# Optimization experiments

Measured on AMD Instinct MI355X. Metric: run time of the kernel, lower is better.

## Reference

```python
import math
import jax, jax.numpy as jnp
import numpy as np

B, T, IN, D, H, L = 128, 1024, 32, 128, 8, 2
U = max(1, min(int(5 * math.log(T + 1)), T))  # ProbSparse sampled queries = 34


def setup_inputs() -> dict:
    key = jax.random.key(0)
    ks = jax.random.split(key, 12)
    def w(k, shape):
        fan_in = shape[-2]
        return jax.random.normal(k, shape, jnp.float32) / jnp.sqrt(jnp.float32(fan_in))
    idx = jnp.stack([jax.random.permutation(jax.random.fold_in(ks[1], l), T)[:U]
                     for l in range(L)]).astype(jnp.int64 if jax.config.jax_enable_x64 else jnp.int32)
    return {
        "x": jax.random.normal(ks[0], (B, T, IN), jnp.float32),
        "idx": idx,
        "proj_w": w(ks[2], (IN, D)), "proj_b": jnp.zeros((D,), jnp.float32),
        "wq": w(ks[3], (L, D, D)), "wk": w(ks[4], (L, D, D)), "wv": w(ks[5], (L, D, D)),
        "wo": w(ks[6], (L, D, D)), "wo_b": jnp.zeros((L, D), jnp.float32),
        "ln1_g": jnp.ones((L, D), jnp.float32), "ln1_b": jnp.zeros((L, D), jnp.float32),
        "ff1_w": w(ks[7], (L, D, 4 * D)), "ff1_b": jnp.zeros((L, 4 * D), jnp.float32),
        "ff2_w": w(ks[8], (L, 4 * D, D)), "ff2_b": jnp.zeros((L, D), jnp.float32),
        "ln2_g": jnp.ones((L, D), jnp.float32), "ln2_b": jnp.zeros((L, D), jnp.float32),
        "head_g": jnp.ones((D,), jnp.float32), "head_bb": jnp.zeros((D,), jnp.float32),
        "head_w": w(ks[9], (D, 1)), "head_wb": jnp.zeros((1,), jnp.float32),
    }


def _ln(x, g, b, eps=1e-5):
    m = x.mean(-1, keepdims=True)
    v = ((x - m) ** 2).mean(-1, keepdims=True)
    return (x - m) / jnp.sqrt(v + eps) * g + b


def _pos_encoding():
    pos = jnp.arange(T, dtype=jnp.float32)[:, None]
    div = jnp.exp(jnp.arange(0, D, 2, dtype=jnp.float32) * (-math.log(10000.0) / D))
    # interleave sin/cos -> [T, D]
    return jnp.stack([jnp.sin(pos * div), jnp.cos(pos * div)], axis=-1).reshape(T, D)


def reference(x, idx, proj_w, proj_b, wq, wk, wv, wo, wo_b, ln1_g, ln1_b,
              ff1_w, ff1_b, ff2_w, ff2_b, ln2_g, ln2_b,
              head_g, head_bb, head_w, head_wb):
    Dh = D // H
    h = x @ proj_w + proj_b + _pos_encoding()[None]  # [B,T,D]
    for l in range(L):
        q = (h @ wq[l]).reshape(B, T, H, Dh).transpose(0, 2, 1, 3)
        k = (h @ wk[l]).reshape(B, T, H, Dh).transpose(0, 2, 1, 3)
        v = (h @ wv[l]).reshape(B, T, H, Dh).transpose(0, 2, 1, 3)
        qs = q[:, :, idx[l], :]  # gather sampled queries [B,H,U,Dh]
        scores = jnp.einsum('bhud,bhtd->bhut', qs, k) / jnp.sqrt(jnp.float32(Dh))
        attn = jax.nn.softmax(scores, axis=-1)
        ctx = jnp.einsum('bhut,bhtd->bhud', attn, v)  # [B,H,U,Dh]
        base = jnp.broadcast_to(ctx.mean(axis=2, keepdims=True), (B, H, T, Dh))
        out = base.at[:, :, idx[l], :].set(ctx)  # scatter back
        attn_out = out.transpose(0, 2, 1, 3).reshape(B, T, D) @ wo[l] + wo_b[l]
        h = _ln(h + attn_out, ln1_g[l], ln1_b[l])
        ff = jax.nn.gelu(h @ ff1_w[l] + ff1_b[l], approximate=False) @ ff2_w[l] + ff2_b[l]
        h = _ln(h + ff, ln2_g[l], ln2_b[l])
    last = _ln(h[:, -1, :], head_g, head_bb)
    return (last @ head_w + head_wb).squeeze(-1)  # [B]
```

## Files before the change

kernel.cpp:

```cpp
#include <hip/hip_runtime.h>
#include <math.h>

constexpr int B  = 128;
constexpr int T  = 1024;
constexpr int IN_DIM = 32;
constexpr int D  = 128;
constexpr int H  = 8;
constexpr int DH = 16;
constexpr int L  = 2;
constexpr int U  = 34;
constexpr int FF = 512;

typedef __attribute__((ext_vector_type(8))) _Float16 f16x8;
typedef __attribute__((ext_vector_type(2))) _Float16 h2;
typedef __attribute__((ext_vector_type(4))) float f32x4;

__device__ __forceinline__ unsigned short f2h(float x) {
  union { _Float16 h; unsigned short u; } v;
  v.h = (_Float16)x;
  return v.u;
}

__device__ __forceinline__ h2 shfl_xor_h2(h2 v, int off) {
  union { h2 h; int i; } u;
  u.h = v;
  u.i = __shfl_xor(u.i, off);
  return u.h;
}

__device__ __forceinline__ float erf_fast(float x) {
  float a = fabsf(x);
  float t = __builtin_amdgcn_rcpf(fmaf(0.3275911f, a, 1.f));
  float y = t * (0.254829592f +
            t * (-0.284496736f +
            t * (1.421413741f +
            t * (-1.453152027f +
            t * 1.061405429f))));
  float r = 1.f - y * __expf(-a * a);
  return copysignf(r, x);
}


__device__ __forceinline__ float blockMax256(float v, float* red) {
  for (int off = 32; off; off >>= 1) v = fmaxf(v, __shfl_down(v, off));
  if ((threadIdx.x & 63) == 0) red[threadIdx.x >> 6] = v;
  __syncthreads();
  v = fmaxf(fmaxf(red[0], red[1]), fmaxf(red[2], red[3]));
  __syncthreads();
  return v;
}

__device__ __forceinline__ float blockSum256(float v, float* red) {
  for (int off = 32; off; off >>= 1) v += __shfl_down(v, off);
  if ((threadIdx.x & 63) == 0) red[threadIdx.x >> 6] = v;
  __syncthreads();
  v = red[0] + red[1] + red[2] + red[3];
  __syncthreads();
  return v;
}


__global__ void k_prep(const float* __restrict__ in, unsigned short* __restrict__ out,
                       int K, int N) {
  int t = blockIdx.x * 256 + threadIdx.x;
  if (t >= K * N) return;
  int n = t / K, k = t - n * K;
  out[t] = f2h(in[(size_t)k * N + n]);
}

__global__ __launch_bounds__(D) void k_proj(const float* __restrict__ x,
                                            const float* __restrict__ pw,
                                            const float* __restrict__ pb,
                                            float* __restrict__ h) {
  int row = blockIdx.x;
  int t = row & (T - 1);
  int d = threadIdx.x;
  __shared__ float xs[IN_DIM];
  if (threadIdx.x < IN_DIM) xs[threadIdx.x] = x[(size_t)row * IN_DIM + threadIdx.x];
  __syncthreads();
  float acc = pb[d];
#pragma unroll
  for (int i = 0; i < IN_DIM; ++i) acc += xs[i] * pw[i * D + d];
  int j = d >> 1;
  float div = expf((float)(2 * j) * (-logf(10000.f) / (float)D));
  float ang = (float)t * div;
  acc += (d & 1) ? cosf(ang) : sinf(ang);
  h[(size_t)row * D + d] = acc;
}

__global__ __launch_bounds__(256) void k_kv_mfma2(
    const float* __restrict__ h,
    const unsigned short* __restrict__ wkt,
    const unsigned short* __restrict__ wvt,
    unsigned short* __restrict__ kbuf, unsigned short* __restrict__ vbuf) {
  __shared__ unsigned short hsb[16 * 128];
  const int tid = threadIdx.x;
  const int r0 = blockIdx.x * 16;
  {
    int m = tid >> 4, kc = tid & 15;
    const float* src = h + (size_t)(r0 + m) * D + kc * 8;
    float4 x0 = *(const float4*)src;
    float4 x1 = *(const float4*)(src + 4);
    f16x8 p;
    p[0] = (_Float16)x0.x; p[1] = (_Float16)x0.y;
    p[2] = (_Float16)x0.z; p[3] = (_Float16)x0.w;
    p[4] = (_Float16)x1.x; p[5] = (_Float16)x1.y;
    p[6] = (_Float16)x1.z; p[7] = (_Float16)x1.w;
    int byte = (m << 8) + (kc << 4);
    byte ^= (m & 7) << 4;
    *(f16x8*)((char*)hsb + byte) = p;
  }
  __syncthreads();
  const int wv = tid >> 6;
  const int l15 = tid & 15;
  const int lq = (tid & 63) >> 4;
  f16x8 afr[4];
#pragma unroll
  for (int ks = 0; ks < 4; ++ks) {
    int byte = (l15 << 8) + ks * 64 + (lq << 4);
    byte ^= (l15 & 7) << 4;
    afr[ks] = *(const f16x8*)((const char*)hsb + byte);
  }
  const unsigned short* wt = (wv < 2) ? wkt : wvt;
  unsigned short* outp = (wv < 2) ? kbuf : vbuf;
  const int cw = (wv & 1) * 64;
  f32x4 acc[4];
#pragma unroll
  for (int nt = 0; nt < 4; ++nt) acc[nt] = (f32x4){0.f, 0.f, 0.f, 0.f};
#pragma unroll
  for (int nt = 0; nt < 4; ++nt) {
    const unsigned short* wp = wt + (size_t)(cw + nt * 16 + l15) * 128 + lq * 8;
#pragma unroll
    for (int ks = 0; ks < 4; ++ks) {
      f16x8 bf = *(const f16x8*)(wp + ks * 32);
      acc[nt] = __builtin_amdgcn_mfma_f32_16x16x32_f16(afr[ks], bf, acc[nt], 0, 0, 0);
    }
  }
#pragma unroll
  for (int nt = 0; nt < 4; ++nt) {
    int col = cw + nt * 16 + l15;
    int hcol = col >> 4, dh = col & 15;
#pragma unroll
    for (int r = 0; r < 4; ++r) {
      int row = r0 + 4 * lq + r;
      int b = row >> 10, t = row & (T - 1);
      outp[(((size_t)b * H + hcol) * T + t) * DH + dh] = f2h(acc[nt][r]);
    }
  }
}

__global__ __launch_bounds__(D) void k_qrow(const float* __restrict__ h,
                                            const int* __restrict__ idx,
                                            const float* __restrict__ wq,
                                            float* __restrict__ qs) {
  int bu = blockIdx.x;
  int b = bu / U, u = bu - b * U;
  int t = idx[u];
  __shared__ float hs[D];
  hs[threadIdx.x] = h[((size_t)b * T + t) * D + threadIdx.x];
  __syncthreads();
  int d = threadIdx.x;
  float acc = 0.f;
  for (int k = 0; k < D; ++k) acc += hs[k] * wq[k * D + d];
  qs[(size_t)bu * D + d] = acc;
}

__global__ __launch_bounds__(256) void k_attn5(const float* __restrict__ qs,
                                               const unsigned short* __restrict__ kbuf,
                                               const unsigned short* __restrict__ vbuf,
                                               float* __restrict__ ctx) {
  constexpr int NWG = B * H * 17;
  int bid = blockIdx.x;
  int orig = (bid & 7) * (NWG / 8) + (bid >> 3);
  int up = orig % 17;
  int gb = orig / 17;
  int hh = gb & 7, b = gb >> 3;
  int u0 = up * 2;

  __shared__ float sc[2][T];
  __shared__ h2 qh[2][8];
  __shared__ float red[4];
  __shared__ float redw[4][2][DH];
  const int tid = threadIdx.x;

  if (tid < 16) {
    int uu = tid >> 3, jj = tid & 7;
    const float* qp = qs + ((size_t)b * U + u0 + uu) * D + hh * DH + jj * 2;
    qh[uu][jj] = (h2){(_Float16)qp[0], (_Float16)qp[1]};
  }
  __syncthreads();
  const unsigned short* kg = kbuf + (size_t)gb * T * DH;
  const unsigned short* vg = vbuf + (size_t)gb * T * DH;

  h2 q0[8], q1[8];
#pragma unroll
  for (int j = 0; j < 8; ++j) { q0[j] = qh[0][j]; q1[j] = qh[1][j]; }

  float lmax0 = -1e30f, lmax1 = -1e30f;
  for (int t = tid; t < T; t += 256) {
    const h2* k2 = (const h2*)(kg + t * DH);
    float s0 = 0.f, s1 = 0.f;
#pragma unroll
    for (int j = 0; j < 8; ++j) {
      h2 kv = k2[j];
      s0 = __builtin_amdgcn_fdot2(q0[j], kv, s0, false);
      s1 = __builtin_amdgcn_fdot2(q1[j], kv, s1, false);
    }
    s0 *= 0.25f; s1 *= 0.25f;
    sc[0][t] = s0; sc[1][t] = s1;
    lmax0 = fmaxf(lmax0, s0);
    lmax1 = fmaxf(lmax1, s1);
  }
  float gmax0 = blockMax256(lmax0, red);
  float gmax1 = blockMax256(lmax1, red);
  float lsum0 = 0.f, lsum1 = 0.f;
  for (int t = tid; t < T; t += 256) {
    float e0 = __expf(sc[0][t] - gmax0);
    float e1 = __expf(sc[1][t] - gmax1);
    sc[0][t] = e0; sc[1][t] = e1;
    lsum0 += e0; lsum1 += e1;
  }
  float inv0 = 1.f / blockSum256(lsum0, red);
  float inv1 = 1.f / blockSum256(lsum1, red);

  h2 p0[8], p1[8];
#pragma unroll
  for (int j = 0; j < 8; ++j) { p0[j] = (h2){0, 0}; p1[j] = (h2){0, 0}; }
  for (int t = tid; t < T; t += 256) {
    const h2* v2 = (const h2*)(vg + t * DH);
    _Float16 a0 = (_Float16)sc[0][t], a1 = (_Float16)sc[1][t];
    h2 a0h = (h2){a0, a0}, a1h = (h2){a1, a1};
#pragma unroll
    for (int j = 0; j < 8; ++j) {
      h2 vv = v2[j];
      p0[j] += a0h * vv;
      p1[j] += a1h * vv;
    }
  }
#pragma unroll
  for (int j = 0; j < 8; ++j) {
#pragma unroll
    for (int off = 32; off; off >>= 1) {
      p0[j] += shfl_xor_h2(p0[j], off);
      p1[j] += shfl_xor_h2(p1[j], off);
    }
  }
  const int wv = tid >> 6, lane = tid & 63;
  if (lane == 0) {
#pragma unroll
    for (int j = 0; j < 8; ++j) {
      redw[wv][0][2 * j]     = (float)p0[j][0];
      redw[wv][0][2 * j + 1] = (float)p0[j][1];
      redw[wv][1][2 * j]     = (float)p1[j][0];
      redw[wv][1][2 * j + 1] = (float)p1[j][1];
    }
  }
  __syncthreads();
  if (tid < 32) {
    int uu = tid >> 4, dh = tid & 15;
    float tot = redw[0][uu][dh] + redw[1][uu][dh] + redw[2][uu][dh] + redw[3][uu][dh];
    float inv = uu ? inv1 : inv0;
    ctx[((size_t)b * U + u0 + uu) * D + hh * DH + dh] = tot * inv;
  }
}

__global__ __launch_bounds__(D) void k_base(const float* __restrict__ ctx,
                                            const float* __restrict__ wo,
                                            const float* __restrict__ wob,
                                            float* __restrict__ baseo) {
  int b = blockIdx.x, d = threadIdx.x;
  __shared__ float bc[D];
  float s = 0.f;
  for (int u = 0; u < U; ++u) s += ctx[((size_t)b * U + u) * D + d];
  bc[d] = s * (1.f / (float)U);
  __syncthreads();
  float acc = wob[d];
  for (int k = 0; k < D; ++k) acc += bc[k] * wo[k * D + d];
  baseo[(size_t)b * D + d] = acc;
}

__global__ __launch_bounds__(D) void k_crow(const float* __restrict__ ctx,
                                            const float* __restrict__ wo,
                                            const float* __restrict__ wob,
                                            float* __restrict__ ctxo) {
  int bu = blockIdx.x, d = threadIdx.x;
  __shared__ float cs[D];
  cs[d] = ctx[(size_t)bu * D + d];
  __syncthreads();
  float acc = wob[d];
  for (int k = 0; k < D; ++k) acc += cs[k] * wo[k * D + d];
  ctxo[(size_t)bu * D + d] = acc;
}

__global__ void k_map(const int* __restrict__ idx, int* __restrict__ map) {
  int t = blockIdx.x * 256 + threadIdx.x;
  if (t >= T) return;
  int m = -1;
  for (int u = 0; u < U; ++u)
    if (idx[u] == t) m = u;
  map[t] = m;
}

__global__ __launch_bounds__(D) void k_ln1(float* __restrict__ h,
                                           const float* __restrict__ ctxo,
                                           const float* __restrict__ baseo,
                                           const int* __restrict__ map,
                                           const float* __restrict__ g,
                                           const float* __restrict__ bb) {
  int row = blockIdx.x;
  int b = row >> 10, t = row & (T - 1);
  int d = threadIdx.x;
  int u = map[t];
  float add = (u >= 0) ? ctxo[((size_t)b * U + u) * D + d]
                       : baseo[(size_t)b * D + d];
  float y = h[(size_t)row * D + d] + add;
  __shared__ float red[2];
  float s = y;
  for (int off = 32; off; off >>= 1) s += __shfl_down(s, off);
  if ((threadIdx.x & 63) == 0) red[threadIdx.x >> 6] = s;
  __syncthreads();
  float m = (red[0] + red[1]) * (1.f / D);
  __syncthreads();
  float e = y - m;
  float v = e * e;
  for (int off = 32; off; off >>= 1) v += __shfl_down(v, off);
  if ((threadIdx.x & 63) == 0) red[threadIdx.x >> 6] = v;
  __syncthreads();
  float inv = rsqrtf((red[0] + red[1]) * (1.f / D) + 1e-5f);
  h[(size_t)row * D + d] = e * inv * g[d] + bb[d];
}

constexpr int RF2 = 32;
__global__ __launch_bounds__(512) void k_ff4(
    const float* __restrict__ h,
    const unsigned short* __restrict__ w1t,
    const float* __restrict__ b1,
    const unsigned short* __restrict__ w2t,
    const float* __restrict__ b2,
    const float* __restrict__ g,
    const float* __restrict__ bb,
    float* __restrict__ hout) {
  __shared__ unsigned short hsb[RF2 * 128];
  __shared__ unsigned short g16[RF2][520];
  __shared__ float mv[RF2][2];

  const int tid = threadIdx.x;
  const int r0 = blockIdx.x * RF2;

  {
    int m = tid >> 4, kc = tid & 15;
    const float* src = h + (size_t)(r0 + m) * D + kc * 8;
    float4 x0 = *(const float4*)src;
    float4 x1 = *(const float4*)(src + 4);
    f16x8 p;
    p[0] = (_Float16)x0.x; p[1] = (_Float16)x0.y;
    p[2] = (_Float16)x0.z; p[3] = (_Float16)x0.w;
    p[4] = (_Float16)x1.x; p[5] = (_Float16)x1.y;
    p[6] = (_Float16)x1.z; p[7] = (_Float16)x1.w;
    int byte = (m << 8) + (kc << 4);
    byte ^= (m & 7) << 4;
    *(f16x8*)((char*)hsb + byte) = p;
  }
  __syncthreads();

  const int wv = tid >> 6;
  const int l15 = tid & 15;
  const int lq = (tid & 63) >> 4;

  f16x8 afr[2][4];
#pragma unroll
  for (int mt = 0; mt < 2; ++mt)
#pragma unroll
    for (int ks = 0; ks < 4; ++ks) {
      int m = mt * 16 + l15;
      int byte = (m << 8) + ks * 64 + (lq << 4);
      byte ^= (m & 7) << 4;
      afr[mt][ks] = *(const f16x8*)((const char*)hsb + byte);
    }

  for (int nt = 0; nt < 4; ++nt) {
    int n0 = wv * 64 + nt * 16;
    const unsigned short* wp = w1t + (size_t)(n0 + l15) * 128 + lq * 8;
    f32x4 a0 = (f32x4){0.f, 0.f, 0.f, 0.f};
    f32x4 a1 = (f32x4){0.f, 0.f, 0.f, 0.f};
#pragma unroll
    for (int ks = 0; ks < 4; ++ks) {
      f16x8 bf = *(const f16x8*)(wp + ks * 32);
      a0 = __builtin_amdgcn_mfma_f32_16x16x32_f16(afr[0][ks], bf, a0, 0, 0, 0);
      a1 = __builtin_amdgcn_mfma_f32_16x16x32_f16(afr[1][ks], bf, a1, 0, 0, 0);
    }
    float bcol = b1[n0 + l15];
#pragma unroll
    for (int r = 0; r < 4; ++r) {
      int row0 = 4 * lq + r;
      float v0 = a0[r] + bcol;
      v0 = 0.5f * v0 * (1.f + erf_fast(v0 * 0.70710678118654752f));
      g16[row0][n0 + l15] = f2h(v0);
      float v1 = a1[r] + bcol;
      v1 = 0.5f * v1 * (1.f + erf_fast(v1 * 0.70710678118654752f));
      g16[row0 + 16][n0 + l15] = f2h(v1);
    }
  }
  __syncthreads();

  f32x4 acc2[2];
  acc2[0] = (f32x4){0.f, 0.f, 0.f, 0.f};
  acc2[1] = (f32x4){0.f, 0.f, 0.f, 0.f};
  const int ncol = wv * 16 + l15;
  const unsigned short* wp2b = w2t + (size_t)ncol * 512;
  for (int ks = 0; ks < 16; ++ks) {
    f16x8 a0 = *(const f16x8*)&g16[l15][ks * 32 + lq * 8];
    f16x8 a1 = *(const f16x8*)&g16[16 + l15][ks * 32 + lq * 8];
    f16x8 bf = *(const f16x8*)(wp2b + ks * 32 + lq * 8);
    acc2[0] = __builtin_amdgcn_mfma_f32_16x16x32_f16(a0, bf, acc2[0], 0, 0, 0);
    acc2[1] = __builtin_amdgcn_mfma_f32_16x16x32_f16(a1, bf, acc2[1], 0, 0, 0);
  }
  __syncthreads();

  float* ys = (float*)&g16[0][0];
  {
    float bc = b2[ncol];
#pragma unroll
    for (int mt = 0; mt < 2; ++mt)
#pragma unroll
      for (int r = 0; r < 4; ++r) {
        int row = mt * 16 + 4 * lq + r;
        ys[row * 128 + ncol] = h[(size_t)(r0 + row) * D + ncol] + acc2[mt][r] + bc;
      }
  }
  __syncthreads();

  {
    int row = tid >> 4, lane16 = tid & 15;
    float s = 0.f;
    for (int dd = lane16; dd < D; dd += 16) s += ys[row * 128 + dd];
    for (int off = 8; off; off >>= 1) s += __shfl_down(s, off, 16);
    if (lane16 == 0) mv[row][0] = s * (1.f / D);
  }
  __syncthreads();
  {
    int row = tid >> 4, lane16 = tid & 15;
    float mu = mv[row][0];
    float v2 = 0.f;
    for (int dd = lane16; dd < D; dd += 16) {
      float e = ys[row * 128 + dd] - mu;
      v2 += e * e;
    }
    for (int off = 8; off; off >>= 1) v2 += __shfl_down(v2, off, 16);
    if (lane16 == 0) mv[row][1] = rsqrtf(v2 * (1.f / D) + 1e-5f);
  }
  __syncthreads();
  for (int i = tid; i < RF2 * D; i += 512) {
    int r = i >> 7, dd = i & 127;
    hout[(size_t)(r0 + r) * D + dd] = (ys[r * 128 + dd] - mv[r][0]) * mv[r][1] * g[dd] + bb[dd];
  }
}

__global__ __launch_bounds__(D) void k_head(const float* __restrict__ h,
                                            const float* __restrict__ g,
                                            const float* __restrict__ bb,
                                            const float* __restrict__ hw,
                                            const float* __restrict__ hwb,
                                            float* __restrict__ out) {
  int b = blockIdx.x, d = threadIdx.x;
  float y = h[((size_t)b * T + (T - 1)) * D + d];
  __shared__ float red[2];
  float s = y;
  for (int off = 32; off; off >>= 1) s += __shfl_down(s, off);
  if ((threadIdx.x & 63) == 0) red[threadIdx.x >> 6] = s;
  __syncthreads();
  float m = (red[0] + red[1]) * (1.f / D);
  __syncthreads();
  float e = y - m;
  float v = e * e;
  for (int off = 32; off; off >>= 1) v += __shfl_down(v, off);
  if ((threadIdx.x & 63) == 0) red[threadIdx.x >> 6] = v;
  __syncthreads();
  float inv = rsqrtf((red[0] + red[1]) * (1.f / D) + 1e-5f);
  __syncthreads();
  float last = e * inv * g[d] + bb[d];
  float p = last * hw[d];
  for (int off = 32; off; off >>= 1) p += __shfl_down(p, off);
  if ((threadIdx.x & 63) == 0) red[threadIdx.x >> 6] = p;
  __syncthreads();
  if (threadIdx.x == 0) out[b] = red[0] + red[1] + hwb[0];
}


extern "C" void kernel_launch(void* const* d_in, const int* in_sizes, int n_in,
                              void* d_out, int out_size, void* d_ws, size_t ws_size,
                              hipStream_t stream) {
  const float* x       = (const float*)d_in[0];
  const int*   idx     = (const int*)d_in[1];
  const float* proj_w  = (const float*)d_in[2];
  const float* proj_b  = (const float*)d_in[3];
  const float* wq      = (const float*)d_in[4];
  const float* wk      = (const float*)d_in[5];
  const float* wv      = (const float*)d_in[6];
  const float* wo      = (const float*)d_in[7];
  const float* wo_b    = (const float*)d_in[8];
  const float* ln1_g   = (const float*)d_in[9];
  const float* ln1_b   = (const float*)d_in[10];
  const float* ff1_w   = (const float*)d_in[11];
  const float* ff1_b   = (const float*)d_in[12];
  const float* ff2_w   = (const float*)d_in[13];
  const float* ff2_b   = (const float*)d_in[14];
  const float* ln2_g   = (const float*)d_in[15];
  const float* ln2_b   = (const float*)d_in[16];
  const float* head_g  = (const float*)d_in[17];
  const float* head_bb = (const float*)d_in[18];
  const float* head_w  = (const float*)d_in[19];
  const float* head_wb = (const float*)d_in[20];
  float* out = (float*)d_out;

  float* wsf  = (float*)d_ws;
  float* h    = wsf;
  float* kreg = h    + (size_t)B * T * D;
  float* vreg = kreg + (size_t)B * T * D;
  float* qs   = vreg + (size_t)B * T * D;
  float* ctx  = qs   + (size_t)B * U * D;
  float* ctxo = ctx  + (size_t)B * U * D;
  float* baseo= ctxo + (size_t)B * U * D;
  int*   map  = (int*)(baseo + (size_t)B * D);
  unsigned short* kbuf16 = (unsigned short*)kreg;
  unsigned short* vbuf16 = (unsigned short*)vreg;
  unsigned short* w1T = (unsigned short*)qs;
  unsigned short* w2T = w1T + 65536;
  unsigned short* wkT = w2T + 65536;
  unsigned short* wvT = wkT + 16384;

  k_proj<<<B * T, D, 0, stream>>>(x, proj_w, proj_b, h);

  for (int l = 0; l < L; ++l) {
    const float* wq_l = wq + (size_t)l * D * D;
    const float* wo_l = wo + (size_t)l * D * D;
    const int*   idx_l = idx + l * U;

    k_prep<<<64, 256, 0, stream>>>(wk + (size_t)l * D * D, wkT, 128, 128);
    k_prep<<<64, 256, 0, stream>>>(wv + (size_t)l * D * D, wvT, 128, 128);
    k_kv_mfma2<<<B * T / 16, 256, 0, stream>>>(h, wkT, wvT, kbuf16, vbuf16);
    k_qrow<<<B * U, D, 0, stream>>>(h, idx_l, wq_l, qs);
    k_attn5<<<B * H * 17, 256, 0, stream>>>(qs, kbuf16, vbuf16, ctx);
    k_base<<<B, D, 0, stream>>>(ctx, wo_l, wo_b + l * D, baseo);
    k_crow<<<B * U, D, 0, stream>>>(ctx, wo_l, wo_b + l * D, ctxo);
    k_map<<<(T + 255) / 256, 256, 0, stream>>>(idx_l, map);
    k_ln1<<<B * T, D, 0, stream>>>(h, ctxo, baseo, map,
                                   ln1_g + l * D, ln1_b + l * D);
    k_prep<<<256, 256, 0, stream>>>(ff1_w + (size_t)l * D * FF, w1T, 128, 512);
    k_prep<<<256, 256, 0, stream>>>(ff2_w + (size_t)l * FF * D, w2T, 512, 128);
    k_ff4<<<B * T / RF2, 512, 0, stream>>>(h, w1T, ff1_b + l * FF,
                                           w2T, ff2_b + l * D,
                                           ln2_g + l * D, ln2_b + l * D, h);
  }

  k_head<<<B, D, 0, stream>>>(h, head_g, head_bb, head_w, head_wb, out);
}
```

Baseline: 881.1 us.

## Fuse weight prep and base/ctx projections, vectorize LN1, split FF2 accumulators

The four per-layer weight transposes are merged into one kernel launched up front for both layers, and the base and ctx output projections are merged into one kernel. LayerNorm1 now processes 8 rows per 256-thread block with float4 loads and wave-level shuffles in place of block-wide syncs. The FF2 MFMA loop uses two independent accumulator chains to shorten dependency stalls, and the positional encoding uses fast intrinsics. Together these cut launch count and LN1 sync overhead, at the cost of a larger workspace, fast-math sin/cos error on large angles, and a changed summation order in FF2.

```diff
diff --git a/kernel.cpp b/kernel.cpp
--- a/kernel.cpp
+++ b/kernel.cpp
@@ -60,12 +60,31 @@
 }
 
 
-__global__ void k_prep(const float* __restrict__ in, unsigned short* __restrict__ out,
-                       int K, int N) {
-  int t = blockIdx.x * 256 + threadIdx.x;
-  if (t >= K * N) return;
-  int n = t / K, k = t - n * K;
-  out[t] = f2h(in[(size_t)k * N + n]);
+__global__ void k_prep_all(const float* __restrict__ wk_l,
+                           const float* __restrict__ wv_l,
+                           const float* __restrict__ w1_l,
+                           const float* __restrict__ w2_l,
+                           unsigned short* __restrict__ wkT,
+                           unsigned short* __restrict__ wvT,
+                           unsigned short* __restrict__ w1T,
+                           unsigned short* __restrict__ w2T) {
+  int idx = blockIdx.x * 256 + threadIdx.x;
+  if (idx < 16384) {
+    int n = idx >> 7, k = idx & 127;
+    wkT[idx] = f2h(wk_l[k * 128 + n]);
+  } else if (idx < 32768) {
+    int j = idx - 16384;
+    int n = j >> 7, k = j & 127;
+    wvT[j] = f2h(wv_l[k * 128 + n]);
+  } else if (idx < 98304) {
+    int j = idx - 32768;
+    int n = j >> 7, k = j & 127;
+    w1T[j] = f2h(w1_l[k * 512 + n]);
+  } else if (idx < 163840) {
+    int j = idx - 98304;
+    int n = j >> 9, k = j & 511;
+    w2T[j] = f2h(w2_l[k * 128 + n]);
+  }
 }
 
 __global__ __launch_bounds__(D) void k_proj(const float* __restrict__ x,
@@ -82,9 +101,9 @@
 #pragma unroll
   for (int i = 0; i < IN_DIM; ++i) acc += xs[i] * pw[i * D + d];
   int j = d >> 1;
-  float div = expf((float)(2 * j) * (-logf(10000.f) / (float)D));
+  float div = __expf((float)(2 * j) * (-logf(10000.f) / (float)D));
   float ang = (float)t * div;
-  acc += (d & 1) ? cosf(ang) : sinf(ang);
+  acc += (d & 1) ? __cosf(ang) : __sinf(ang);
   h[(size_t)row * D + d] = acc;
 }
 
@@ -264,32 +283,27 @@
   }
 }
 
-__global__ __launch_bounds__(D) void k_base(const float* __restrict__ ctx,
-                                            const float* __restrict__ wo,
-                                            const float* __restrict__ wob,
-                                            float* __restrict__ baseo) {
-  int b = blockIdx.x, d = threadIdx.x;
-  __shared__ float bc[D];
-  float s = 0.f;
-  for (int u = 0; u < U; ++u) s += ctx[((size_t)b * U + u) * D + d];
-  bc[d] = s * (1.f / (float)U);
-  __syncthreads();
-  float acc = wob[d];
-  for (int k = 0; k < D; ++k) acc += bc[k] * wo[k * D + d];
-  baseo[(size_t)b * D + d] = acc;
-}
-
-__global__ __launch_bounds__(D) void k_crow(const float* __restrict__ ctx,
-                                            const float* __restrict__ wo,
-                                            const float* __restrict__ wob,
-                                            float* __restrict__ ctxo) {
-  int bu = blockIdx.x, d = threadIdx.x;
+__global__ __launch_bounds__(D) void k_bc(const float* __restrict__ ctx,
+                                          const float* __restrict__ wo,
+                                          const float* __restrict__ wob,
+                                          float* __restrict__ ctxo,
+                                          float* __restrict__ baseo) {
+  int i = blockIdx.x;
+  int b = i / (U + 1), u = i - b * (U + 1);
+  int d = threadIdx.x;
   __shared__ float cs[D];
-  cs[d] = ctx[(size_t)bu * D + d];
+  if (u < U) {
+    cs[d] = ctx[((size_t)b * U + u) * D + d];
+  } else {
+    float s = 0.f;
+    for (int uu = 0; uu < U; ++uu) s += ctx[((size_t)b * U + uu) * D + d];
+    cs[d] = s * (1.f / (float)U);
+  }
   __syncthreads();
   float acc = wob[d];
   for (int k = 0; k < D; ++k) acc += cs[k] * wo[k * D + d];
-  ctxo[(size_t)bu * D + d] = acc;
+  if (u < U) ctxo[((size_t)b * U + u) * D + d] = acc;
+  else       baseo[(size_t)b * D + d] = acc;
 }
 
 __global__ void k_map(const int* __restrict__ idx, int* __restrict__ map) {
@@ -301,33 +315,41 @@
   map[t] = m;
 }
 
-__global__ __launch_bounds__(D) void k_ln1(float* __restrict__ h,
-                                           const float* __restrict__ ctxo,
-                                           const float* __restrict__ baseo,
-                                           const int* __restrict__ map,
-                                           const float* __restrict__ g,
-                                           const float* __restrict__ bb) {
-  int row = blockIdx.x;
+__global__ __launch_bounds__(256) void k_ln1v(float* __restrict__ h,
+                                              const float* __restrict__ ctxo,
+                                              const float* __restrict__ baseo,
+                                              const int* __restrict__ map,
+                                              const float* __restrict__ g,
+                                              const float* __restrict__ bb) {
+  const int tid = threadIdx.x;
+  int sub = tid >> 5;
+  int lane32 = tid & 31;
+  int row = blockIdx.x * 8 + sub;
   int b = row >> 10, t = row & (T - 1);
-  int d = threadIdx.x;
   int u = map[t];
-  float add = (u >= 0) ? ctxo[((size_t)b * U + u) * D + d]
-                       : baseo[(size_t)b * D + d];
-  float y = h[(size_t)row * D + d] + add;
-  __shared__ float red[2];
-  float s = y;
-  for (int off = 32; off; off >>= 1) s += __shfl_down(s, off);
-  if ((threadIdx.x & 63) == 0) red[threadIdx.x >> 6] = s;
-  __syncthreads();
-  float m = (red[0] + red[1]) * (1.f / D);
-  __syncthreads();
-  float e = y - m;
-  float v = e * e;
-  for (int off = 32; off; off >>= 1) v += __shfl_down(v, off);
-  if ((threadIdx.x & 63) == 0) red[threadIdx.x >> 6] = v;
-  __syncthreads();
-  float inv = rsqrtf((red[0] + red[1]) * (1.f / D) + 1e-5f);
-  h[(size_t)row * D + d] = e * inv * g[d] + bb[d];
+  const float* src = (u >= 0) ? ctxo + ((size_t)b * U + u) * D
+                              : baseo + (size_t)b * D;
+  float4 add = *(const float4*)(src + lane32 * 4);
+  float4 hv  = *(const float4*)(h + (size_t)row * D + lane32 * 4);
+  float4 y;
+  y.x = hv.x + add.x; y.y = hv.y + add.y; y.z = hv.z + add.z; y.w = hv.w + add.w;
+  float s = y.x + y.y + y.z + y.w;
+#pragma unroll
+  for (int off = 16; off; off >>= 1) s += __shfl_xor(s, off, 32);
+  float mu = s * (1.f / D);
+  float ex = y.x - mu, ey = y.y - mu, ez = y.z - mu, ew = y.w - mu;
+  float v2 = ex * ex + ey * ey + ez * ez + ew * ew;
+#pragma unroll
+  for (int off = 16; off; off >>= 1) v2 += __shfl_xor(v2, off, 32);
+  float inv = rsqrtf(v2 * (1.f / D) + 1e-5f);
+  float4 gv = *(const float4*)(g + lane32 * 4);
+  float4 bv = *(const float4*)(bb + lane32 * 4);
+  float4 o;
+  o.x = ex * inv * gv.x + bv.x;
+  o.y = ey * inv * gv.y + bv.y;
+  o.z = ez * inv * gv.z + bv.z;
+  o.w = ew * inv * gv.w + bv.w;
+  *(float4*)(h + (size_t)row * D + lane32 * 4) = o;
 }
 
 constexpr int RF2 = 32;
@@ -403,17 +425,34 @@
   }
   __syncthreads();
 
-  f32x4 acc2[2];
-  acc2[0] = (f32x4){0.f, 0.f, 0.f, 0.f};
-  acc2[1] = (f32x4){0.f, 0.f, 0.f, 0.f};
+  f32x4 a2a[2], a2b[2];
+  a2a[0] = (f32x4){0.f, 0.f, 0.f, 0.f};
+  a2a[1] = (f32x4){0.f, 0.f, 0.f, 0.f};
+  a2b[0] = (f32x4){0.f, 0.f, 0.f, 0.f};
+  a2b[1] = (f32x4){0.f, 0.f, 0.f, 0.f};
   const int ncol = wv * 16 + l15;
   const unsigned short* wp2b = w2t + (size_t)ncol * 512;
-  for (int ks = 0; ks < 16; ++ks) {
-    f16x8 a0 = *(const f16x8*)&g16[l15][ks * 32 + lq * 8];
-    f16x8 a1 = *(const f16x8*)&g16[16 + l15][ks * 32 + lq * 8];
-    f16x8 bf = *(const f16x8*)(wp2b + ks * 32 + lq * 8);
-    acc2[0] = __builtin_amdgcn_mfma_f32_16x16x32_f16(a0, bf, acc2[0], 0, 0, 0);
-    acc2[1] = __builtin_amdgcn_mfma_f32_16x16x32_f16(a1, bf, acc2[1], 0, 0, 0);
+  for (int ks = 0; ks < 8; ++ks) {
+    int k0 = ks * 32 + lq * 8;
+    int k1 = (ks + 8) * 32 + lq * 8;
+    f16x8 x0 = *(const f16x8*)&g16[l15][k0];
+    f16x8 x1 = *(const f16x8*)&g16[16 + l15][k0];
+    f16x8 w0 = *(const f16x8*)(wp2b + k0);
+    a2a[0] = __builtin_amdgcn_mfma_f32_16x16x32_f16(x0, w0, a2a[0], 0, 0, 0);
+    a2a[1] = __builtin_amdgcn_mfma_f32_16x16x32_f16(x1, w0, a2a[1], 0, 0, 0);
+    f16x8 y0 = *(const f16x8*)&g16[l15][k1];
+    f16x8 y1 = *(const f16x8*)&g16[16 + l15][k1];
+    f16x8 w1 = *(const f16x8*)(wp2b + k1);
+    a2b[0] = __builtin_amdgcn_mfma_f32_16x16x32_f16(y0, w1, a2b[0], 0, 0, 0);
+    a2b[1] = __builtin_amdgcn_mfma_f32_16x16x32_f16(y1, w1, a2b[1], 0, 0, 0);
+  }
+  f32x4 acc2[2];
+#pragma unroll
+  for (int mt = 0; mt < 2; ++mt) {
+    acc2[mt][0] = a2a[mt][0] + a2b[mt][0];
+    acc2[mt][1] = a2a[mt][1] + a2b[mt][1];
+    acc2[mt][2] = a2a[mt][2] + a2b[mt][2];
+    acc2[mt][3] = a2a[mt][3] + a2b[mt][3];
   }
   __syncthreads();
 
@@ -524,10 +563,20 @@
   int*   map  = (int*)(baseo + (size_t)B * D);
   unsigned short* kbuf16 = (unsigned short*)kreg;
   unsigned short* vbuf16 = (unsigned short*)vreg;
-  unsigned short* w1T = (unsigned short*)qs;
-  unsigned short* w2T = w1T + 65536;
-  unsigned short* wkT = w2T + 65536;
-  unsigned short* wvT = wkT + 16384;
+  unsigned short* wbuf = (unsigned short*)(map + 1024);
+  const size_t PL = 16384 + 16384 + 65536 + 65536;
+
+  for (int l = 0; l < L; ++l) {
+    unsigned short* wkT = wbuf + (size_t)l * PL;
+    unsigned short* wvT = wkT + 16384;
+    unsigned short* w1T = wvT + 16384;
+    unsigned short* w2T = w1T + 65536;
+    k_prep_all<<<640, 256, 0, stream>>>(wk + (size_t)l * D * D,
+                                        wv + (size_t)l * D * D,
+                                        ff1_w + (size_t)l * D * FF,
+                                        ff2_w + (size_t)l * FF * D,
+                                        wkT, wvT, w1T, w2T);
+  }
 
   k_proj<<<B * T, D, 0, stream>>>(x, proj_w, proj_b, h);
 
@@ -535,19 +584,18 @@
     const float* wq_l = wq + (size_t)l * D * D;
     const float* wo_l = wo + (size_t)l * D * D;
     const int*   idx_l = idx + l * U;
-
-    k_prep<<<64, 256, 0, stream>>>(wk + (size_t)l * D * D, wkT, 128, 128);
-    k_prep<<<64, 256, 0, stream>>>(wv + (size_t)l * D * D, wvT, 128, 128);
+    unsigned short* wkT = wbuf + (size_t)l * PL;
+    unsigned short* wvT = wkT + 16384;
+    unsigned short* w1T = wvT + 16384;
+    unsigned short* w2T = w1T + 65536;
+
     k_kv_mfma2<<<B * T / 16, 256, 0, stream>>>(h, wkT, wvT, kbuf16, vbuf16);
     k_qrow<<<B * U, D, 0, stream>>>(h, idx_l, wq_l, qs);
     k_attn5<<<B * H * 17, 256, 0, stream>>>(qs, kbuf16, vbuf16, ctx);
-    k_base<<<B, D, 0, stream>>>(ctx, wo_l, wo_b + l * D, baseo);
-    k_crow<<<B * U, D, 0, stream>>>(ctx, wo_l, wo_b + l * D, ctxo);
+    k_bc<<<B * (U + 1), D, 0, stream>>>(ctx, wo_l, wo_b + l * D, ctxo, baseo);
     k_map<<<(T + 255) / 256, 256, 0, stream>>>(idx_l, map);
-    k_ln1<<<B * T, D, 0, stream>>>(h, ctxo, baseo, map,
-                                   ln1_g + l * D, ln1_b + l * D);
-    k_prep<<<256, 256, 0, stream>>>(ff1_w + (size_t)l * D * FF, w1T, 128, 512);
-    k_prep<<<256, 256, 0, stream>>>(ff2_w + (size_t)l * FF * D, w2T, 512, 128);
+    k_ln1v<<<B * T / 8, 256, 0, stream>>>(h, ctxo, baseo, map,
+                                          ln1_g + l * D, ln1_b + l * D);
     k_ff4<<<B * T / RF2, 512, 0, stream>>>(h, w1T, ff1_b + l * FF,
                                            w2T, ff2_b + l * D,
                                            ln2_g + l * D, ln2_b + l * D, h);
```

After: 797.6 us. 1.1x faster.
